# Kernel optimization log

Hardware: AMD Instinct MI355X
Metric: run time of the kernel (lower is better)

## Reference

```python
import jax, jax.numpy as jnp
import numpy as np

K = 9          # neighbors kept after dilation
DILATION = 2   # top-k runs with K*DILATION then strided slice
EPS = 1e-12    # F.normalize eps


def setup_inputs() -> dict:
    key = jax.random.key(0)
    # x: [B, C, N, 1] feature map over N points with C channels
    x = jax.random.normal(key, (2, 64, 8192, 1), dtype=jnp.float32)
    return {"x": x}


def reference(x):
    k_total = K * DILATION
    # L2-normalize along channel dim (F.normalize(x, p=2, dim=1))
    norm = jnp.sqrt(jnp.sum(x * x, axis=1, keepdims=True))
    xn = x / jnp.maximum(norm, EPS)
    # [B, C, N, 1] -> [B, N, C]
    pts = jnp.transpose(jnp.squeeze(xn, -1), (0, 2, 1))
    B, N, _ = pts.shape
    # pairwise squared distances: ||xi||^2 - 2 xi.xj + ||xj||^2  -> [B, N, N]
    sq = jnp.sum(pts * pts, axis=-1, keepdims=True)            # [B, N, 1]
    dist = sq - 2.0 * jnp.einsum('bnc,bmc->bnm', pts, pts) + jnp.swapaxes(sq, 1, 2)
    # k nearest = top-k of negated distance (matches torch.topk(-dist, k))
    _, nn_idx = jax.lax.top_k(-dist, k_total)                  # [B, N, k_total] int32
    center_idx = jnp.broadcast_to(jnp.arange(N, dtype=nn_idx.dtype)[None, :, None],
                                  (B, N, k_total))
    edge_index = jnp.stack([nn_idx, center_idx], axis=0)       # [2, B, N, k_total]
    # dilation (non-stochastic path): strided slice over neighbor dim
    return edge_index[:, :, :, ::DILATION]                     # [2, B, N, K]
```

## Files before the change

### kernel.cpp

```cpp
#include <hip/hip_runtime.h>


#define NPTS  8192
#define CHN   64
#define NB    2
#define KF    18
#define KC    8
#define KM    20
#define KOUT  9

typedef unsigned u32;
typedef unsigned short u16;
typedef unsigned long long u64;
typedef __attribute__((ext_vector_type(4))) unsigned u32x4;
typedef __attribute__((ext_vector_type(8))) short bf16x8;
typedef __attribute__((ext_vector_type(4))) float f32x4;

__device__ __forceinline__ u32 umin32(u32 a, u32 b) { return a < b ? a : b; }
__device__ __forceinline__ u32 umax32(u32 a, u32 b) { return a > b ? a : b; }

__device__ __forceinline__ u32 pack_split(float v) {
  const u32 hv = __float_as_uint(v) & 0xffff0000u;
  const float lo = v - __uint_as_float(hv);
  return hv | (__float_as_uint(lo) >> 16);
}

__device__ __forceinline__ u32 mono32(float f) {
  const u32 u = __float_as_uint(f);
  const u32 s = (u32)((int)u >> 31);
  return u ^ (s | 0x80000000u);
}

template <int KK>
__device__ __forceinline__ void insmm(u32 key, u32 (&d)[KK]) {
#pragma unroll
  for (int k = KK - 1; k >= 1; --k) d[k] = umax32(d[k - 1], umin32(d[k], key));
  d[0] = umin32(d[0], key);
}

template <int KK>
__device__ __forceinline__ void ins64(u64 key, u64 (&d)[KK]) {
  if (key < d[KK - 1]) {
#pragma unroll
    for (int k = KK - 1; k >= 1; --k) {
      const bool up = d[k - 1] > key;
      const bool here = (!up) && (d[k] > key);
      d[k] = up ? d[k - 1] : (here ? key : d[k]);
    }
    if (d[0] > key) d[0] = key;
  }
}

__device__ __forceinline__ void unpack_pair(u32x4 r0, u32x4 r1,
                                            bf16x8& fh, bf16x8& fl) {
  u32x4 h, l;
  h.x = (r0.x >> 16) | (r0.y & 0xffff0000u);
  h.y = (r0.z >> 16) | (r0.w & 0xffff0000u);
  h.z = (r1.x >> 16) | (r1.y & 0xffff0000u);
  h.w = (r1.z >> 16) | (r1.w & 0xffff0000u);
  l.x = (r0.x & 0xffffu) | (r0.y << 16);
  l.y = (r0.z & 0xffffu) | (r0.w << 16);
  l.z = (r1.x & 0xffffu) | (r1.y << 16);
  l.w = (r1.z & 0xffffu) | (r1.w << 16);
  fh = __builtin_bit_cast(bf16x8, h);
  fl = __builtin_bit_cast(bf16x8, l);
}

__global__ __launch_bounds__(128) void prep_kernel(
    const float* __restrict__ x, float* __restrict__ pts, float* __restrict__ sq) {
  const int b = blockIdx.x >> 6;
  const int n = ((blockIdx.x & 63) << 7) + threadIdx.x;
  const float* __restrict__ xb = x + (size_t)b * CHN * NPTS + n;
  float v[CHN];
  float ss = 0.f;
#pragma unroll
  for (int c = 0; c < CHN; ++c) {
    v[c] = xb[(size_t)c * NPTS];
    ss = __fadd_rn(ss, __fmul_rn(v[c], v[c]));
  }
  const float den = fmaxf(__fsqrt_rn(ss), 1e-12f);
#pragma unroll
  for (int c = 0; c < CHN; ++c) v[c] = __fdiv_rn(v[c], den);
  float r[8];
#pragma unroll
  for (int j = 0; j < 8; ++j) r[j] = __fmul_rn(v[j], v[j]);
#pragma unroll
  for (int blk = 1; blk < 8; ++blk)
#pragma unroll
    for (int j = 0; j < 8; ++j)
      r[j] = __fadd_rn(r[j], __fmul_rn(v[8 * blk + j], v[8 * blk + j]));
  const float t0 = __fadd_rn(r[0], r[1]);
  const float t1 = __fadd_rn(r[2], r[3]);
  const float t2 = __fadd_rn(r[4], r[5]);
  const float t3 = __fadd_rn(r[6], r[7]);
  sq[(b << 13) + n] = __fadd_rn(__fadd_rn(t0, t1), __fadd_rn(t2, t3));
  float4* dst = (float4*)(pts + (size_t)(b * NPTS + n) * CHN);
#pragma unroll
  for (int u = 0; u < 16; ++u)
    dst[u] = make_float4(v[4 * u], v[4 * u + 1], v[4 * u + 2], v[4 * u + 3]);
}

__global__ __launch_bounds__(256, 3) void knn_part_kernel(
    const float* __restrict__ pts, const float* __restrict__ sq,
    u16* __restrict__ cand) {
  __shared__ __align__(16) u32 pp[2][4096];
  __shared__ __align__(16) u32 dtu[4352];
  __shared__ float sqp[2][64];

  const int tid = threadIdx.x;
  const int vb = ((blockIdx.x & 7) * 96) + (blockIdx.x >> 3);
  const int part = vb >> 8;
  const int w = vb & 255;
  const int b = w >> 7;
  const int qbase = (w & 127) << 6;
  const int t_lo = part * 43;
  const int t_hi = (part == 2) ? 128 : (t_lo + 43);
  const float* __restrict__ pb = pts + ((size_t)b << 19);
  const float* __restrict__ sqb = sq + (b << 13);

  const int sr = tid >> 2, ssub = tid & 3;
  const int lane = tid & 63, wid = tid >> 6;
  const int qoff = (wid & 1) << 5;
  const int moff = (wid >> 1) << 5;
  const int l15 = lane & 15;
  const int h4 = lane >> 4;

  {
    const float4* qsrc =
        (const float4*)(pb + ((size_t)(qbase + sr) << 6) + (ssub << 4));
    const float4* psrc =
        (const float4*)(pb + ((size_t)t_lo << 12) + (sr << 6) + (ssub << 4));
    u32* qw = dtu + (sr << 6);
    u32* pw = pp[0] + (sr << 6);
#pragma unroll
    for (int q = 0; q < 4; ++q) {
      const float4 qv = qsrc[q];
      const float4 pv = psrc[q];
      u32x4 a, c;
      a.x = pack_split(qv.x); a.y = pack_split(qv.y);
      a.z = pack_split(qv.z); a.w = pack_split(qv.w);
      c.x = pack_split(pv.x); c.y = pack_split(pv.y);
      c.z = pack_split(pv.z); c.w = pack_split(pv.w);
      const int wofs = ((ssub << 4) + (q << 2)) ^ ((sr & 15) << 2);
      *(u32x4*)(qw + wofs) = a;
      *(u32x4*)(pw + wofs) = c;
    }
    if (tid < 64) sqp[0][tid] = sqb[(t_lo << 6) + tid];
  }
  __syncthreads();

  bf16x8 ah[2][2], al[2][2];
#pragma unroll
  for (int g = 0; g < 2; ++g)
#pragma unroll
    for (int s = 0; s < 2; ++s) {
      const int row = qoff + (g << 4) + l15;
      const int w0 = (s << 5) + (h4 << 3);
      const u32* base = dtu + row * 64;
      const u32x4 r0 = *(const u32x4*)(base + (w0 ^ (l15 << 2)));
      const u32x4 r1 = *(const u32x4*)(base + ((w0 + 4) ^ (l15 << 2)));
      unpack_pair(r0, r1, ah[g][s], al[g][s]);
    }
  __syncthreads();

  u32 d[2][4][KC];
#pragma unroll
  for (int g = 0; g < 2; ++g)
#pragma unroll
    for (int i = 0; i < 4; ++i)
#pragma unroll
      for (int k = 0; k < KC; ++k) d[g][i][k] = 0xffffffffu;

  for (int t = t_lo; t < t_hi; ++t) {
    const int cur = (t - t_lo) & 1;
    float4 st[4];
    float sqv = 0.f;
    const bool more = (t + 1) < t_hi;
    if (more) {
      const float4* nsrc = (const float4*)(pb + ((size_t)(t + 1) << 12) +
                                           (sr << 6) + (ssub << 4));
#pragma unroll
      for (int q = 0; q < 4; ++q) st[q] = nsrc[q];
      if (tid < 64) sqv = sqb[((t + 1) << 6) + tid];
    }
    const u32* ppc = pp[cur];
    const int lbase = (t - t_lo) << 6;
#pragma unroll
    for (int f = 0; f < 2; ++f) {
      const int m_l = moff + (f << 4) + l15;
      const float sqm = sqp[cur][m_l];
      f32x4 acc[2];
      acc[0] = (f32x4){0.f, 0.f, 0.f, 0.f};
      acc[1] = acc[0];
#pragma unroll
      for (int s = 0; s < 2; ++s) {
        const int w0 = (s << 5) + (h4 << 3);
        const u32* base = ppc + m_l * 64;
        const u32x4 r0 = *(const u32x4*)(base + (w0 ^ (l15 << 2)));
        const u32x4 r1 = *(const u32x4*)(base + ((w0 + 4) ^ (l15 << 2)));
        bf16x8 bh, bl;
        unpack_pair(r0, r1, bh, bl);
        acc[0] = __builtin_amdgcn_mfma_f32_16x16x32_bf16(ah[0][s], bh, acc[0], 0, 0, 0);
        acc[1] = __builtin_amdgcn_mfma_f32_16x16x32_bf16(ah[1][s], bh, acc[1], 0, 0, 0);
        acc[0] = __builtin_amdgcn_mfma_f32_16x16x32_bf16(al[0][s], bh, acc[0], 0, 0, 0);
        acc[1] = __builtin_amdgcn_mfma_f32_16x16x32_bf16(al[1][s], bh, acc[1], 0, 0, 0);
        acc[0] = __builtin_amdgcn_mfma_f32_16x16x32_bf16(ah[0][s], bl, acc[0], 0, 0, 0);
        acc[1] = __builtin_amdgcn_mfma_f32_16x16x32_bf16(ah[1][s], bl, acc[1], 0, 0, 0);
      }
      const u32 lidx = (u32)(lbase + m_l);
#pragma unroll
      for (int g = 0; g < 2; ++g)
#pragma unroll
        for (int i = 0; i < 4; ++i) {
          const float dist = fmaf(-2.f, acc[g][i], sqm);
          const u32 key = (mono32(dist) & 0xfffff000u) | lidx;
          insmm<KC>(key, d[g][i]);
        }
    }
    if (more) {
      u32* wp = pp[cur ^ 1] + (sr << 6);
#pragma unroll
      for (int q = 0; q < 4; ++q) {
        u32x4 pk;
        pk.x = pack_split(st[q].x); pk.y = pack_split(st[q].y);
        pk.z = pack_split(st[q].z); pk.w = pack_split(st[q].w);
        *(u32x4*)(wp + (((ssub << 4) + (q << 2)) ^ ((sr & 15) << 2))) = pk;
      }
      if (tid < 64) sqp[cur ^ 1][tid] = sqv;
    }
    __syncthreads();
  }

  u32* mg = (u32*)pp;
  const int rowc_b = ((wid & 1) << 4) + (h4 << 2);
  const int stream = ((wid >> 1) << 4) + l15;
  for (int chunk = 0; chunk < 2; ++chunk) {
#pragma unroll
    for (int i = 0; i < 4; ++i) {
      const int cb = (((rowc_b + i) << 5) + stream) << 1;
      u32x4 lo4, hi4;
      lo4.x = d[chunk][i][0]; lo4.y = d[chunk][i][1];
      lo4.z = d[chunk][i][2]; lo4.w = d[chunk][i][3];
      hi4.x = d[chunk][i][4]; hi4.y = d[chunk][i][5];
      hi4.z = d[chunk][i][6]; hi4.w = d[chunk][i][7];
      *(u32x4*)(mg + ((cb ^ h4) << 2)) = lo4;
      *(u32x4*)(mg + (((cb + 1) ^ h4) << 2)) = hi4;
    }
    __syncthreads();
    {
      const int rowc = tid >> 3, oct = tid & 7;
      u32 m1[14];
#pragma unroll
      for (int k = 0; k < 14; ++k) m1[k] = 0xffffffffu;
      const u32* rd = mg + ((rowc << 6) + (oct << 3) << 2);
#pragma unroll
      for (int j = 0; j < 8; ++j) {
        const int jj = (j + tid) & 7;
        const u32x4 k4 = *(const u32x4*)(rd + (jj << 2));
        insmm<14>(k4.x, m1);
        insmm<14>(k4.y, m1);
        insmm<14>(k4.z, m1);
        insmm<14>(k4.w, m1);
      }
      u32* wr = dtu + rowc * 112 + oct * 14;
#pragma unroll
      for (int k = 0; k < 14; ++k) wr[k] = m1[k];
    }
    __syncthreads();
    if (tid < 64) {
      const int rowc = tid >> 1, half = tid & 1;
      u32 m2[KM];
#pragma unroll
      for (int k = 0; k < KM; ++k) m2[k] = 0xffffffffu;
      const u32* rd = dtu + rowc * 112 + half * 56;
      for (int j = 0; j < 56; ++j) insmm<KM>(rd[j], m2);
      u32* wr = mg + rowc * 40 + half * KM;
#pragma unroll
      for (int k = 0; k < KM; ++k) wr[k] = m2[k];
    }
    __syncthreads();
    if (tid < 32) {
      u32 m3[KM];
#pragma unroll
      for (int k = 0; k < KM; ++k) m3[k] = 0xffffffffu;
      const u32* rd = mg + tid * 40;
      for (int j = 0; j < 40; ++j) insmm<KM>(rd[j], m3);
      const int row = ((tid >> 4) << 5) + (chunk << 4) + (tid & 15);
      const int rg = (b << 13) + qbase + row;
      u16* cw = cand + (size_t)rg * 60 + part * KM;
#pragma unroll
      for (int k = 0; k < KM; ++k)
        cw[k] = (u16)((t_lo << 6) + (m3[k] & 0xfffu));
    }
    __syncthreads();
  }
}

__global__ __launch_bounds__(256) void finalize_kernel(
    const float* __restrict__ pts, const float* __restrict__ sq,
    const u16* __restrict__ cand, int* __restrict__ out) {
  __shared__ u64 ex[64 * 60];
  const int tid = threadIdx.x;
  const int rl = tid >> 2, sub = tid & 3;
  const int row = blockIdx.x * 64 + rl;
  const int b = row >> 13;
  const int n = row & 8191;
  const float* __restrict__ qrow = pts + ((size_t)row << 6);
  const float sqn = sq[row];
  const u16* __restrict__ cr = cand + (size_t)row * 60 + sub * 15;
  for (int j = 0; j < 15; ++j) {
    const int ix = cr[j];
    const float* __restrict__ pv = pts + ((size_t)((b << 13) + ix) << 6);
    float dot = 0.f;
#pragma unroll
    for (int c = 0; c < CHN; ++c)
      dot = __fadd_rn(dot, __fmul_rn(qrow[c], pv[c]));
    const float dist =
        __fadd_rn(__fsub_rn(sqn, __fmul_rn(2.0f, dot)), sq[(b << 13) + ix]);
    ex[rl * 60 + sub * 15 + j] = ((u64)mono32(dist) << 32) | (unsigned)ix;
  }
  __syncthreads();
  if (tid < 64) {
    u64 m18[KF];
#pragma unroll
    for (int k = 0; k < KF; ++k) m18[k] = ~0ull;
    for (int j = 0; j < 60; ++j) ins64<KF>(ex[tid * 60 + j], m18);
    const int row2 = blockIdx.x * 64 + tid;
    const int n2 = row2 & 8191;
    int* o0 = out + (size_t)row2 * KOUT;
    int* o1 = o0 + NB * NPTS * KOUT;
#pragma unroll
    for (int k = 0; k < KOUT; ++k) {
      o0[k] = (int)(m18[2 * k] & 0xffffffffu);
      o1[k] = n2;
    }
  }
}

extern "C" void kernel_launch(void* const* d_in, const int* in_sizes, int n_in,
                              void* d_out, int out_size, void* d_ws, size_t ws_size,
                              hipStream_t stream) {
  const float* x = (const float*)d_in[0];
  float* pts = (float*)d_ws;
  float* sqg = pts + (size_t)NB * NPTS * CHN;
  u16* cand = (u16*)(sqg + NB * NPTS);
  int* out = (int*)d_out;
  prep_kernel<<<dim3(128), dim3(128), 0, stream>>>(x, pts, sqg);
  knn_part_kernel<<<dim3(768), dim3(256), 0, stream>>>(pts, sqg, cand);
  finalize_kernel<<<dim3(256), dim3(256), 0, stream>>>(pts, sqg, cand, out);
}
```

Measured before the change: 245.3 us.

## Store split bf16 hi/lo planes in LDS and fold distance into MFMA accumulator

Candidates are now pre-split into separate bf16 high and low planes in shared memory, so MFMA operands load directly without per-iteration unpack shuffles. The dtu buffer is removed. The query is negated and the accumulator is seeded with (sq+2)/2, which makes the raw accumulator bits a monotone key and drops the fma and mono32 per element. The candidate range is split into 4 parts of 32 tiles instead of 3, with 1024 blocks and occupancy 4. Finalize rescoring grows to 80 candidates per row. The exchange is more candidate rescoring and a changed merge layout that may add LDS bank conflicts.

Result: slower. 549.6 us (+124.1%).

```diff
diff --git a/kernel.cpp b/kernel.cpp
--- a/kernel.cpp
+++ b/kernel.cpp
@@ -8,6 +8,8 @@
 #define KC    8
 #define KM    20
 #define KOUT  9
+#define NPART 4
+#define TPB   32
 
 typedef unsigned u32;
 typedef unsigned short u16;
@@ -19,10 +21,17 @@
 __device__ __forceinline__ u32 umin32(u32 a, u32 b) { return a < b ? a : b; }
 __device__ __forceinline__ u32 umax32(u32 a, u32 b) { return a > b ? a : b; }
 
-__device__ __forceinline__ u32 pack_split(float v) {
-  const u32 hv = __float_as_uint(v) & 0xffff0000u;
-  const float lo = v - __uint_as_float(hv);
-  return hv | (__float_as_uint(lo) >> 16);
+__device__ __forceinline__ void split4(float4 v, u32* h, u32* l) {
+  const u32 b0 = __float_as_uint(v.x), b1 = __float_as_uint(v.y);
+  const u32 b2 = __float_as_uint(v.z), b3 = __float_as_uint(v.w);
+  const float l0 = v.x - __uint_as_float(b0 & 0xffff0000u);
+  const float l1 = v.y - __uint_as_float(b1 & 0xffff0000u);
+  const float l2 = v.z - __uint_as_float(b2 & 0xffff0000u);
+  const float l3 = v.w - __uint_as_float(b3 & 0xffff0000u);
+  h[0] = __builtin_amdgcn_perm(b1, b0, 0x07060302u);
+  h[1] = __builtin_amdgcn_perm(b3, b2, 0x07060302u);
+  l[0] = __builtin_amdgcn_perm(__float_as_uint(l1), __float_as_uint(l0), 0x07060302u);
+  l[1] = __builtin_amdgcn_perm(__float_as_uint(l3), __float_as_uint(l2), 0x07060302u);
 }
 
 __device__ __forceinline__ u32 mono32(float f) {
@@ -49,21 +58,6 @@
     }
     if (d[0] > key) d[0] = key;
   }
-}
-
-__device__ __forceinline__ void unpack_pair(u32x4 r0, u32x4 r1,
-                                            bf16x8& fh, bf16x8& fl) {
-  u32x4 h, l;
-  h.x = (r0.x >> 16) | (r0.y & 0xffff0000u);
-  h.y = (r0.z >> 16) | (r0.w & 0xffff0000u);
-  h.z = (r1.x >> 16) | (r1.y & 0xffff0000u);
-  h.w = (r1.z >> 16) | (r1.w & 0xffff0000u);
-  l.x = (r0.x & 0xffffu) | (r0.y << 16);
-  l.y = (r0.z & 0xffffu) | (r0.w << 16);
-  l.z = (r1.x & 0xffffu) | (r1.y << 16);
-  l.w = (r1.z & 0xffffu) | (r1.w << 16);
-  fh = __builtin_bit_cast(bf16x8, h);
-  fl = __builtin_bit_cast(bf16x8, l);
 }
 
 __global__ __launch_bounds__(128) void prep_kernel(
@@ -100,21 +94,19 @@
     dst[u] = make_float4(v[4 * u], v[4 * u + 1], v[4 * u + 2], v[4 * u + 3]);
 }
 
-__global__ __launch_bounds__(256, 3) void knn_part_kernel(
+__global__ __launch_bounds__(256, 4) void knn_part_kernel(
     const float* __restrict__ pts, const float* __restrict__ sq,
     u16* __restrict__ cand) {
   __shared__ __align__(16) u32 pp[2][4096];
-  __shared__ __align__(16) u32 dtu[4352];
   __shared__ float sqp[2][64];
 
   const int tid = threadIdx.x;
-  const int vb = ((blockIdx.x & 7) * 96) + (blockIdx.x >> 3);
+  const int vb = ((blockIdx.x & 7) << 7) + (blockIdx.x >> 3);
   const int part = vb >> 8;
   const int w = vb & 255;
   const int b = w >> 7;
   const int qbase = (w & 127) << 6;
-  const int t_lo = part * 43;
-  const int t_hi = (part == 2) ? 128 : (t_lo + 43);
+  const int t_lo = part << 5;
   const float* __restrict__ pb = pts + ((size_t)b << 19);
   const float* __restrict__ sqb = sq + (b << 13);
 
@@ -124,28 +116,32 @@
   const int moff = (wid >> 1) << 5;
   const int l15 = lane & 15;
   const int h4 = lane >> 4;
+  const int sw = l15 & 7;
 
   {
     const float4* qsrc =
         (const float4*)(pb + ((size_t)(qbase + sr) << 6) + (ssub << 4));
     const float4* psrc =
-        (const float4*)(pb + ((size_t)t_lo << 12) + (sr << 6) + (ssub << 4));
-    u32* qw = dtu + (sr << 6);
-    u32* pw = pp[0] + (sr << 6);
+        (const float4*)(pb + ((size_t)((t_lo << 6) + sr) << 6) + (ssub << 4));
+    u32 qh[8], ql[8], ph[8], pl[8];
 #pragma unroll
     for (int q = 0; q < 4; ++q) {
-      const float4 qv = qsrc[q];
-      const float4 pv = psrc[q];
-      u32x4 a, c;
-      a.x = pack_split(qv.x); a.y = pack_split(qv.y);
-      a.z = pack_split(qv.z); a.w = pack_split(qv.w);
-      c.x = pack_split(pv.x); c.y = pack_split(pv.y);
-      c.z = pack_split(pv.z); c.w = pack_split(pv.w);
-      const int wofs = ((ssub << 4) + (q << 2)) ^ ((sr & 15) << 2);
-      *(u32x4*)(qw + wofs) = a;
-      *(u32x4*)(pw + wofs) = c;
-    }
-    if (tid < 64) sqp[0][tid] = sqb[(t_lo << 6) + tid];
+      float4 qv = qsrc[q];
+      qv.x = -qv.x; qv.y = -qv.y; qv.z = -qv.z; qv.w = -qv.w;
+      split4(qv, qh + 2 * q, ql + 2 * q);
+      split4(psrc[q], ph + 2 * q, pl + 2 * q);
+    }
+    const int qa = sr * 32 + (((ssub << 1) ^ (sr & 7)) << 2);
+    const int qb2 = sr * 32 + ((((ssub << 1) + 1) ^ (sr & 7)) << 2);
+    *(u32x4*)(pp[1] + qa) = *(u32x4*)qh;
+    *(u32x4*)(pp[1] + qb2) = *(u32x4*)(qh + 4);
+    *(u32x4*)(pp[1] + 2048 + qa) = *(u32x4*)ql;
+    *(u32x4*)(pp[1] + 2048 + qb2) = *(u32x4*)(ql + 4);
+    *(u32x4*)(pp[0] + qa) = *(u32x4*)ph;
+    *(u32x4*)(pp[0] + qb2) = *(u32x4*)(ph + 4);
+    *(u32x4*)(pp[0] + 2048 + qa) = *(u32x4*)pl;
+    *(u32x4*)(pp[0] + 2048 + qb2) = *(u32x4*)(pl + 4);
+    if (tid < 64) sqp[0][tid] = (sqb[(t_lo << 6) + tid] + 2.f) * 0.5f;
   }
   __syncthreads();
 
@@ -155,11 +151,9 @@
 #pragma unroll
     for (int s = 0; s < 2; ++s) {
       const int row = qoff + (g << 4) + l15;
-      const int w0 = (s << 5) + (h4 << 3);
-      const u32* base = dtu + row * 64;
-      const u32x4 r0 = *(const u32x4*)(base + (w0 ^ (l15 << 2)));
-      const u32x4 r1 = *(const u32x4*)(base + ((w0 + 4) ^ (l15 << 2)));
-      unpack_pair(r0, r1, ah[g][s], al[g][s]);
+      const int off = row * 32 + ((((s << 2) + h4) ^ sw) << 2);
+      ah[g][s] = __builtin_bit_cast(bf16x8, *(const u32x4*)(pp[1] + off));
+      al[g][s] = __builtin_bit_cast(bf16x8, *(const u32x4*)(pp[1] + 2048 + off));
     }
   __syncthreads();
 
@@ -171,35 +165,31 @@
 #pragma unroll
       for (int k = 0; k < KC; ++k) d[g][i][k] = 0xffffffffu;
 
-  for (int t = t_lo; t < t_hi; ++t) {
-    const int cur = (t - t_lo) & 1;
+  for (int tau = 0; tau < TPB; ++tau) {
+    const int cur = tau & 1;
     float4 st[4];
     float sqv = 0.f;
-    const bool more = (t + 1) < t_hi;
+    const bool more = (tau + 1) < TPB;
     if (more) {
-      const float4* nsrc = (const float4*)(pb + ((size_t)(t + 1) << 12) +
-                                           (sr << 6) + (ssub << 4));
+      const float4* nsrc = (const float4*)(
+          pb + ((size_t)(t_lo + tau + 1) << 12) + (sr << 6) + (ssub << 4));
 #pragma unroll
       for (int q = 0; q < 4; ++q) st[q] = nsrc[q];
-      if (tid < 64) sqv = sqb[((t + 1) << 6) + tid];
+      if (tid < 64) sqv = sqb[((t_lo + tau + 1) << 6) + tid];
     }
     const u32* ppc = pp[cur];
-    const int lbase = (t - t_lo) << 6;
 #pragma unroll
     for (int f = 0; f < 2; ++f) {
       const int m_l = moff + (f << 4) + l15;
       const float sqm = sqp[cur][m_l];
       f32x4 acc[2];
-      acc[0] = (f32x4){0.f, 0.f, 0.f, 0.f};
+      acc[0] = (f32x4){sqm, sqm, sqm, sqm};
       acc[1] = acc[0];
 #pragma unroll
       for (int s = 0; s < 2; ++s) {
-        const int w0 = (s << 5) + (h4 << 3);
-        const u32* base = ppc + m_l * 64;
-        const u32x4 r0 = *(const u32x4*)(base + (w0 ^ (l15 << 2)));
-        const u32x4 r1 = *(const u32x4*)(base + ((w0 + 4) ^ (l15 << 2)));
-        bf16x8 bh, bl;
-        unpack_pair(r0, r1, bh, bl);
+        const u32* hb = ppc + m_l * 32 + ((((s << 2) + h4) ^ sw) << 2);
+        const bf16x8 bh = __builtin_bit_cast(bf16x8, *(const u32x4*)hb);
+        const bf16x8 bl = __builtin_bit_cast(bf16x8, *(const u32x4*)(hb + 2048));
         acc[0] = __builtin_amdgcn_mfma_f32_16x16x32_bf16(ah[0][s], bh, acc[0], 0, 0, 0);
         acc[1] = __builtin_amdgcn_mfma_f32_16x16x32_bf16(ah[1][s], bh, acc[1], 0, 0, 0);
         acc[0] = __builtin_amdgcn_mfma_f32_16x16x32_bf16(al[0][s], bh, acc[0], 0, 0, 0);
@@ -207,90 +197,95 @@
         acc[0] = __builtin_amdgcn_mfma_f32_16x16x32_bf16(ah[0][s], bl, acc[0], 0, 0, 0);
         acc[1] = __builtin_amdgcn_mfma_f32_16x16x32_bf16(ah[1][s], bl, acc[1], 0, 0, 0);
       }
-      const u32 lidx = (u32)(lbase + m_l);
+      const u32 lidx = (u32)((tau << 6) + m_l);
 #pragma unroll
       for (int g = 0; g < 2; ++g)
 #pragma unroll
         for (int i = 0; i < 4; ++i) {
-          const float dist = fmaf(-2.f, acc[g][i], sqm);
-          const u32 key = (mono32(dist) & 0xfffff000u) | lidx;
+          const u32 key = (__float_as_uint(acc[g][i]) & 0xfffff000u) | lidx;
           insmm<KC>(key, d[g][i]);
         }
     }
     if (more) {
-      u32* wp = pp[cur ^ 1] + (sr << 6);
-#pragma unroll
-      for (int q = 0; q < 4; ++q) {
-        u32x4 pk;
-        pk.x = pack_split(st[q].x); pk.y = pack_split(st[q].y);
-        pk.z = pack_split(st[q].z); pk.w = pack_split(st[q].w);
-        *(u32x4*)(wp + (((ssub << 4) + (q << 2)) ^ ((sr & 15) << 2))) = pk;
-      }
-      if (tid < 64) sqp[cur ^ 1][tid] = sqv;
-    }
-    __syncthreads();
-  }
-
-  u32* mg = (u32*)pp;
-  const int rowc_b = ((wid & 1) << 4) + (h4 << 2);
+      u32 hh[8], ll[8];
+#pragma unroll
+      for (int q = 0; q < 4; ++q) split4(st[q], hh + 2 * q, ll + 2 * q);
+      u32* wp = pp[cur ^ 1];
+      const int qa = sr * 32 + (((ssub << 1) ^ (sr & 7)) << 2);
+      const int qb2 = sr * 32 + ((((ssub << 1) + 1) ^ (sr & 7)) << 2);
+      *(u32x4*)(wp + qa) = *(u32x4*)hh;
+      *(u32x4*)(wp + qb2) = *(u32x4*)(hh + 4);
+      *(u32x4*)(wp + 2048 + qa) = *(u32x4*)ll;
+      *(u32x4*)(wp + 2048 + qb2) = *(u32x4*)(ll + 4);
+      if (tid < 64) sqp[cur ^ 1][tid] = (sqv + 2.f) * 0.5f;
+    }
+    __syncthreads();
+  }
+
+  u32* mg = &pp[0][0];
   const int stream = ((wid >> 1) << 4) + l15;
+  const int rcb = ((wid & 1) << 4) + (h4 << 2);
+#pragma unroll
   for (int chunk = 0; chunk < 2; ++chunk) {
 #pragma unroll
     for (int i = 0; i < 4; ++i) {
-      const int cb = (((rowc_b + i) << 5) + stream) << 1;
-      u32x4 lo4, hi4;
-      lo4.x = d[chunk][i][0]; lo4.y = d[chunk][i][1];
-      lo4.z = d[chunk][i][2]; lo4.w = d[chunk][i][3];
-      hi4.x = d[chunk][i][4]; hi4.y = d[chunk][i][5];
-      hi4.z = d[chunk][i][6]; hi4.w = d[chunk][i][7];
-      *(u32x4*)(mg + ((cb ^ h4) << 2)) = lo4;
-      *(u32x4*)(mg + (((cb + 1) ^ h4) << 2)) = hi4;
+      u32* wr = mg + ((rcb + i) * 32 + stream) * 8;
+      u32x4 a, c;
+      a.x = d[chunk][i][0]; a.y = d[chunk][i][1];
+      a.z = d[chunk][i][2]; a.w = d[chunk][i][3];
+      c.x = d[chunk][i][4]; c.y = d[chunk][i][5];
+      c.z = d[chunk][i][6]; c.w = d[chunk][i][7];
+      *(u32x4*)wr = a;
+      *(u32x4*)(wr + 4) = c;
     }
     __syncthreads();
     {
       const int rowc = tid >> 3, oct = tid & 7;
+      u32* base = mg + rowc * 256 + oct * 32;
       u32 m1[14];
 #pragma unroll
       for (int k = 0; k < 14; ++k) m1[k] = 0xffffffffu;
-      const u32* rd = mg + ((rowc << 6) + (oct << 3) << 2);
 #pragma unroll
       for (int j = 0; j < 8; ++j) {
-        const int jj = (j + tid) & 7;
-        const u32x4 k4 = *(const u32x4*)(rd + (jj << 2));
+        const u32x4 k4 = *(const u32x4*)(base + (j << 2));
         insmm<14>(k4.x, m1);
         insmm<14>(k4.y, m1);
         insmm<14>(k4.z, m1);
         insmm<14>(k4.w, m1);
       }
-      u32* wr = dtu + rowc * 112 + oct * 14;
-#pragma unroll
-      for (int k = 0; k < 14; ++k) wr[k] = m1[k];
+#pragma unroll
+      for (int k = 0; k < 14; ++k) base[k] = m1[k];
     }
     __syncthreads();
     if (tid < 64) {
       const int rowc = tid >> 1, half = tid & 1;
+      u32* rb = mg + rowc * 256 + half * 128;
       u32 m2[KM];
 #pragma unroll
       for (int k = 0; k < KM; ++k) m2[k] = 0xffffffffu;
-      const u32* rd = dtu + rowc * 112 + half * 56;
-      for (int j = 0; j < 56; ++j) insmm<KM>(rd[j], m2);
-      u32* wr = mg + rowc * 40 + half * KM;
-#pragma unroll
-      for (int k = 0; k < KM; ++k) wr[k] = m2[k];
+#pragma unroll
+      for (int o = 0; o < 4; ++o) {
+        const u32* p = rb + o * 32;
+        for (int j = 0; j < 14; ++j) insmm<KM>(p[j], m2);
+      }
+#pragma unroll
+      for (int k = 0; k < KM; ++k) rb[k] = m2[k];
     }
     __syncthreads();
     if (tid < 32) {
       u32 m3[KM];
 #pragma unroll
       for (int k = 0; k < KM; ++k) m3[k] = 0xffffffffu;
-      const u32* rd = mg + tid * 40;
-      for (int j = 0; j < 40; ++j) insmm<KM>(rd[j], m3);
+      const u32* p0 = mg + tid * 256;
+      for (int j = 0; j < KM; ++j) insmm<KM>(p0[j], m3);
+      const u32* p1 = mg + tid * 256 + 128;
+      for (int j = 0; j < KM; ++j) insmm<KM>(p1[j], m3);
       const int row = ((tid >> 4) << 5) + (chunk << 4) + (tid & 15);
       const int rg = (b << 13) + qbase + row;
-      u16* cw = cand + (size_t)rg * 60 + part * KM;
+      u16* cw = cand + (size_t)rg * (NPART * KM) + part * KM;
 #pragma unroll
       for (int k = 0; k < KM; ++k)
-        cw[k] = (u16)((t_lo << 6) + (m3[k] & 0xfffu));
+        cw[k] = (u16)((part << 11) + (m3[k] & 0xfffu));
     }
     __syncthreads();
   }
@@ -299,16 +294,15 @@
 __global__ __launch_bounds__(256) void finalize_kernel(
     const float* __restrict__ pts, const float* __restrict__ sq,
     const u16* __restrict__ cand, int* __restrict__ out) {
-  __shared__ u64 ex[64 * 60];
+  __shared__ u64 ex[64 * 80];
   const int tid = threadIdx.x;
   const int rl = tid >> 2, sub = tid & 3;
   const int row = blockIdx.x * 64 + rl;
   const int b = row >> 13;
-  const int n = row & 8191;
   const float* __restrict__ qrow = pts + ((size_t)row << 6);
   const float sqn = sq[row];
-  const u16* __restrict__ cr = cand + (size_t)row * 60 + sub * 15;
-  for (int j = 0; j < 15; ++j) {
+  const u16* __restrict__ cr = cand + (size_t)row * 80 + sub * 20;
+  for (int j = 0; j < 20; ++j) {
     const int ix = cr[j];
     const float* __restrict__ pv = pts + ((size_t)((b << 13) + ix) << 6);
     float dot = 0.f;
@@ -317,14 +311,14 @@
       dot = __fadd_rn(dot, __fmul_rn(qrow[c], pv[c]));
     const float dist =
         __fadd_rn(__fsub_rn(sqn, __fmul_rn(2.0f, dot)), sq[(b << 13) + ix]);
-    ex[rl * 60 + sub * 15 + j] = ((u64)mono32(dist) << 32) | (unsigned)ix;
+    ex[rl * 80 + sub * 20 + j] = ((u64)mono32(dist) << 32) | (unsigned)ix;
   }
   __syncthreads();
   if (tid < 64) {
     u64 m18[KF];
 #pragma unroll
     for (int k = 0; k < KF; ++k) m18[k] = ~0ull;
-    for (int j = 0; j < 60; ++j) ins64<KF>(ex[tid * 60 + j], m18);
+    for (int j = 0; j < 80; ++j) ins64<KF>(ex[tid * 80 + j], m18);
     const int row2 = blockIdx.x * 64 + tid;
     const int n2 = row2 & 8191;
     int* o0 = out + (size_t)row2 * KOUT;
@@ -346,6 +340,6 @@
   u16* cand = (u16*)(sqg + NB * NPTS);
   int* out = (int*)d_out;
   prep_kernel<<<dim3(128), dim3(128), 0, stream>>>(x, pts, sqg);
-  knn_part_kernel<<<dim3(768), dim3(256), 0, stream>>>(pts, sqg, cand);
+  knn_part_kernel<<<dim3(1024), dim3(256), 0, stream>>>(pts, sqg, cand);
   finalize_kernel<<<dim3(256), dim3(256), 0, stream>>>(pts, sqg, cand, out);
 }
```
